# Optimization experiments

Measured on AMD Instinct MI355X. Metric: run time of the kernel, lower is better.

## Reference

```python
import jax, jax.numpy as jnp
import numpy as np

VOCAB, H, L, NUM_LABELS = 32000, 512, 5, 20


def setup_inputs() -> dict:
    key = jax.random.key(0)
    ks = jax.random.split(key, 8)
    B, T = 64, 512
    inputs = jax.random.randint(ks[0], (B, T), 0, VOCAB, dtype=jnp.int32)
    s = 1.0 / np.sqrt(H)
    emb = jax.random.normal(ks[1], (VOCAB, H), jnp.float32) * 0.02
    emb = emb.at[0].set(0.0)  # padding_idx=0
    W_ih = jax.random.uniform(ks[2], (L, 4 * H, H), jnp.float32, -s, s)
    W_hh = jax.random.uniform(ks[3], (L, 4 * H, H), jnp.float32, -s, s)
    b_ih = jax.random.uniform(ks[4], (L, 4 * H), jnp.float32, -s, s)
    b_hh = jax.random.uniform(ks[5], (L, 4 * H), jnp.float32, -s, s)
    W_cls = jax.random.uniform(ks[6], (NUM_LABELS, H), jnp.float32, -s, s)
    b_cls = jax.random.uniform(ks[7], (NUM_LABELS,), jnp.float32, -s, s)
    return {"inputs": inputs, "emb": emb, "W_ih": W_ih, "W_hh": W_hh,
            "b_ih": b_ih, "b_hh": b_hh, "W_cls": W_cls, "b_cls": b_cls}


def _lstm_layer(x, Wih, Whh, bih, bhh):
    # x: [B, T, H] -> [B, T, H]. PyTorch gate order: i, f, g, o.
    B, T, Hd = x.shape
    xg = jnp.einsum('bth,gh->btg', x, Wih) + bih + bhh  # precompute input gates [B,T,4H]

    def step(carry, xt):
        h, c = carry
        g = xt + h @ Whh.T
        i, f, gg, o = jnp.split(g, 4, axis=-1)
        c = jax.nn.sigmoid(f) * c + jax.nn.sigmoid(i) * jnp.tanh(gg)
        h = jax.nn.sigmoid(o) * jnp.tanh(c)
        return (h, c), h

    h0 = jnp.zeros((B, Hd), x.dtype)
    (_, _), ys = jax.lax.scan(step, (h0, h0), jnp.swapaxes(xg, 0, 1))
    return jnp.swapaxes(ys, 0, 1)


def reference(inputs, emb, W_ih, W_hh, b_ih, b_hh, W_cls, b_cls):
    # Dropout between layers is inactive in eval mode; omitted (deterministic baseline).
    x = emb[inputs]  # [B, T, H]
    for l in range(W_ih.shape[0]):
        x = _lstm_layer(x, W_ih[l], W_hh[l], b_ih[l], b_hh[l])
    feature = x[:, -1]  # last timestep hidden of top layer
    return feature @ W_cls.T + b_cls
```

## Files before the change

kernel.cpp:

```cpp
#include <hip/hip_runtime.h>
#include <cmath>

#define BB 64
#define TT 512
#define HH 512
#define GG 2048
#define TCH 64
#define LDT 132

template<bool GATHER>
__global__ __launch_bounds__(256) void xg_gemm(
    const float* __restrict__ Xsrc, const int* __restrict__ tok,
    const float* __restrict__ Wih, const float* __restrict__ bih,
    const float* __restrict__ bhh, float* __restrict__ XG, int t0)
{
  __shared__ float As[32 * LDT];
  __shared__ float Bs[32 * LDT];
  const int tid = threadIdx.x;
  const int tc = tid & 15, tr = tid >> 4;
  const int m0 = blockIdx.x * 128;
  const int g0 = blockIdx.y * 128;

  float acc[8][8];
#pragma unroll
  for (int i = 0; i < 8; ++i)
#pragma unroll
    for (int j = 0; j < 8; ++j) acc[i][j] = 0.f;

  float4 ra[4], rb[4];
#pragma unroll
  for (int i = 0; i < 4; ++i) {
    const int f = tid + i * 256;
    ra[i] = *(const float4*)&Wih[(size_t)(g0 + (f >> 3)) * HH + ((f & 7) << 2)];
  }
#pragma unroll
  for (int i = 0; i < 4; ++i) {
    const int f = tid + i * 256;
    if (GATHER) {
      const int m = m0 + (f >> 3);
      const int tok_i = tok[(m & 63) * TT + t0 + (m >> 6)];
      rb[i] = *(const float4*)&Xsrc[(size_t)tok_i * HH + ((f & 7) << 2)];
    } else {
      rb[i] = *(const float4*)&Xsrc[((size_t)(t0 + (m0 >> 6) + (f >> 9)) * HH
                                     + ((f >> 4) & 31)) * BB + ((f & 15) << 2)];
    }
  }

  for (int kt = 0; kt < 16; ++kt) {
#pragma unroll
    for (int i = 0; i < 4; ++i) {
      const int f = tid + i * 256;
      const int row = f >> 3, c4 = f & 7, s = c4 & 3;
      const int col = (((row >> 2) ^ s) << 2) + (row & 3);
      As[(c4 * 4 + 0) * LDT + col] = ra[i].x;
      As[(c4 * 4 + 1) * LDT + col] = ra[i].y;
      As[(c4 * 4 + 2) * LDT + col] = ra[i].z;
      As[(c4 * 4 + 3) * LDT + col] = ra[i].w;
    }
#pragma unroll
    for (int i = 0; i < 4; ++i) {
      const int f = tid + i * 256;
      if (GATHER) {
        const int row = f >> 3, c4 = f & 7, s = c4 & 3;
        const int col = (((row >> 2) ^ s) << 2) + (row & 3);
        Bs[(c4 * 4 + 0) * LDT + col] = rb[i].x;
        Bs[(c4 * 4 + 1) * LDT + col] = rb[i].y;
        Bs[(c4 * 4 + 2) * LDT + col] = rb[i].z;
        Bs[(c4 * 4 + 3) * LDT + col] = rb[i].w;
      } else {
        const int kk = (f >> 4) & 31, s = (kk >> 2) & 3;
        const int mq = (((f >> 9) << 4) + (f & 15)) ^ s;
        *(float4*)&Bs[kk * LDT + (mq << 2)] = rb[i];
      }
    }
    __syncthreads();
    if (kt < 15) {
      const int k0 = (kt + 1) * 32;
#pragma unroll
      for (int i = 0; i < 4; ++i) {
        const int f = tid + i * 256;
        ra[i] = *(const float4*)&Wih[(size_t)(g0 + (f >> 3)) * HH + k0 + ((f & 7) << 2)];
      }
#pragma unroll
      for (int i = 0; i < 4; ++i) {
        const int f = tid + i * 256;
        if (GATHER) {
          const int m = m0 + (f >> 3);
          const int tok_i = tok[(m & 63) * TT + t0 + (m >> 6)];
          rb[i] = *(const float4*)&Xsrc[(size_t)tok_i * HH + k0 + ((f & 7) << 2)];
        } else {
          rb[i] = *(const float4*)&Xsrc[((size_t)(t0 + (m0 >> 6) + (f >> 9)) * HH
                                         + k0 + ((f >> 4) & 31)) * BB + ((f & 15) << 2)];
        }
      }
    }
#pragma unroll
    for (int k = 0; k < 32; ++k) {
      const int s = (k >> 2) & 3;
      const float4 a0 = *(const float4*)&As[k * LDT + ((tr ^ s) << 2)];
      const float4 a1 = *(const float4*)&As[k * LDT + ((16 + (tr ^ s)) << 2)];
      const float4 b0 = *(const float4*)&Bs[k * LDT + ((tc ^ s) << 2)];
      const float4 b1 = *(const float4*)&Bs[k * LDT + ((16 + (tc ^ s)) << 2)];
      const float av[8] = {a0.x, a0.y, a0.z, a0.w, a1.x, a1.y, a1.z, a1.w};
      const float bv[8] = {b0.x, b0.y, b0.z, b0.w, b1.x, b1.y, b1.z, b1.w};
#pragma unroll
      for (int i2 = 0; i2 < 8; ++i2)
#pragma unroll
        for (int j2 = 0; j2 < 8; ++j2)
          acc[i2][j2] = fmaf(av[i2], bv[j2], acc[i2][j2]);
    }
    __syncthreads();
  }

#pragma unroll
  for (int ah = 0; ah < 2; ++ah)
#pragma unroll
    for (int i = 0; i < 4; ++i) {
      const int gc = g0 + ah * 64 + tr * 4 + i;
      const float bias = bih[gc] + bhh[gc];
#pragma unroll
      for (int bh = 0; bh < 2; ++bh) {
        const int tl_ = (m0 >> 6) + bh;
        float4 v;
        v.x = acc[ah * 4 + i][bh * 4 + 0] + bias;
        v.y = acc[ah * 4 + i][bh * 4 + 1] + bias;
        v.z = acc[ah * 4 + i][bh * 4 + 2] + bias;
        v.w = acc[ah * 4 + i][bh * 4 + 3] + bias;
        *(float4*)&XG[((size_t)tl_ * GG + gc) * BB + (tc << 2)] = v;
      }
    }
}

__device__ __forceinline__ float4 ld4a(const float* src) {
  const unsigned long long* p = (const unsigned long long*)src;
  const unsigned long long a = __hip_atomic_load(p + 0, __ATOMIC_RELAXED, __HIP_MEMORY_SCOPE_AGENT);
  const unsigned long long b = __hip_atomic_load(p + 1, __ATOMIC_RELAXED, __HIP_MEMORY_SCOPE_AGENT);
  float4 v;
  v.x = __uint_as_float((unsigned)a);
  v.y = __uint_as_float((unsigned)(a >> 32));
  v.z = __uint_as_float((unsigned)b);
  v.w = __uint_as_float((unsigned)(b >> 32));
  return v;
}

__global__ __launch_bounds__(256, 1) void lstm_chunk(
    const float* __restrict__ XG, const float* __restrict__ Whh,
    float* __restrict__ h0, float* __restrict__ h1,
    float* __restrict__ c, float* __restrict__ Y,
    unsigned* __restrict__ flag, int t0, int l)
{
  const int tid = threadIdx.x;
  const int grp = blockIdx.x & 7;
  const int mid = blockIdx.x >> 3;
  const int rp = tid >> 3;
  const int ks = tid & 7;
  const int lr0 = 2 * rp, lr1 = 2 * rp + 1;
  const int gc0 = ((lr0 >> 4) << 9) + mid * 16 + (lr0 & 15);
  const int gc1 = ((lr1 >> 4) << 9) + mid * 16 + (lr1 & 15);

  __shared__ float4 hs4[8 * 136];
  __shared__ float gs[512];

  float4 w0[16], w1[16];
#pragma unroll
  for (int cc = 0; cc < 16; ++cc) {
    w0[cc] = *(const float4*)&Whh[(size_t)gc0 * HH + ks * 64 + cc * 4];
    w1[cc] = *(const float4*)&Whh[(size_t)gc1 * HH + ks * 64 + cc * 4];
  }

  const int hc_l = tid >> 3;
  const int bb_l = tid & 7;
  const int hc_own = mid * 16 + hc_l;
  const int Bg_own = 8 * grp + bb_l;
  float creg = 0.f;
  if (t0 > 0 && tid < 128) creg = c[(size_t)hc_own * BB + Bg_own];

  const int sb = tid >> 7;
  const int sc4 = tid & 127;
  const int lds_i = sc4 + (sc4 >> 4);

  for (int tl = 0; tl < TCH; ++tl) {
    const int t = t0 + tl;
    const int first = (t == 0) ? 1 : 0;
    const float* h_in = (t & 1) ? h1 : h0;
    float* h_out = (t & 1) ? h0 : h1;

    float xgv[4];
    if (tid < 128) {
#pragma unroll
      for (int q = 0; q < 4; ++q)
        xgv[q] = XG[((size_t)tl * GG + (q << 9) + hc_own) * BB + Bg_own];
    }

    if (!first) {
      const float* s0 = &h_in[(size_t)(8 * grp + sb + 0) * HH + (sc4 << 2)];
      const float* s1 = &h_in[(size_t)(8 * grp + sb + 2) * HH + (sc4 << 2)];
      const float* s2 = &h_in[(size_t)(8 * grp + sb + 4) * HH + (sc4 << 2)];
      const float* s3 = &h_in[(size_t)(8 * grp + sb + 6) * HH + (sc4 << 2)];
      float4 va = ld4a(s0);
      float4 vb = ld4a(s1);
      hs4[(sb + 0) * 136 + lds_i] = va;
      va = ld4a(s2);
      hs4[(sb + 2) * 136 + lds_i] = vb;
      vb = ld4a(s3);
      hs4[(sb + 4) * 136 + lds_i] = va;
      hs4[(sb + 6) * 136 + lds_i] = vb;
      __syncthreads();

      float p0[8], p1[8];
#pragma unroll
      for (int b = 0; b < 8; ++b) { p0[b] = 0.f; p1[b] = 0.f; }
#pragma unroll
      for (int cc = 0; cc < 16; ++cc) {
#pragma unroll
        for (int b = 0; b < 8; ++b) {
          const float4 hv = hs4[b * 136 + 17 * ks + cc];
          p0[b] += hv.x * w0[cc].x + hv.y * w0[cc].y + hv.z * w0[cc].z + hv.w * w0[cc].w;
          p1[b] += hv.x * w1[cc].x + hv.y * w1[cc].y + hv.z * w1[cc].z + hv.w * w1[cc].w;
        }
      }
#pragma unroll
      for (int b = 0; b < 8; ++b) {
        float v0 = p0[b], v1 = p1[b];
        v0 += __shfl_xor(v0, 1, 64); v0 += __shfl_xor(v0, 2, 64); v0 += __shfl_xor(v0, 4, 64);
        v1 += __shfl_xor(v1, 1, 64); v1 += __shfl_xor(v1, 2, 64); v1 += __shfl_xor(v1, 4, 64);
        p0[b] = v0; p1[b] = v1;
      }
      if (ks == 0) {
#pragma unroll
        for (int b = 0; b < 8; ++b) {
          gs[lr0 * 8 + b] = p0[b];
          gs[lr1 * 8 + b] = p1[b];
        }
      }
    }
    __syncthreads();

    float hn = 0.f;
    if (tid < 128) {
      float gv[4];
#pragma unroll
      for (int q = 0; q < 4; ++q) {
        float x = xgv[q];
        if (!first) x += gs[(q * 16 + hc_l) * 8 + bb_l];
        gv[q] = x;
      }
      const float cold = first ? 0.f : creg;
      const float si = 1.f / (1.f + expf(-gv[0]));
      const float sf = 1.f / (1.f + expf(-gv[1]));
      const float so = 1.f / (1.f + expf(-gv[3]));
      const float cn = sf * cold + si * tanhf(gv[2]);
      hn = so * tanhf(cn);
      creg = cn;
      __hip_atomic_store(&h_out[(size_t)Bg_own * HH + hc_own], hn,
                         __ATOMIC_RELAXED, __HIP_MEMORY_SCOPE_AGENT);
    }

    asm volatile("s_waitcnt vmcnt(0)" ::: "memory");
    __syncthreads();
    const unsigned sid = (unsigned)(l * TT + t + 1);
    if (tid == 0)
      __hip_atomic_store(&flag[(grp << 5) + mid], sid,
                         __ATOMIC_RELAXED, __HIP_MEMORY_SCOPE_AGENT);
    if (tid < 128)
      Y[((size_t)t * HH + hc_own) * BB + Bg_own] = hn;
    if (tid < 32) {
      const unsigned* fp = &flag[(grp << 5) + tid];
      while (__hip_atomic_load(fp, __ATOMIC_RELAXED, __HIP_MEMORY_SCOPE_AGENT) < sid)
        __builtin_amdgcn_s_sleep(2);
    }
    __syncthreads();
  }

  if (tid < 128) c[(size_t)hc_own * BB + Bg_own] = creg;
}

__global__ __launch_bounds__(64) void cls_kernel(
    const float* __restrict__ Y, const float* __restrict__ Wcls,
    const float* __restrict__ bcls, float* __restrict__ out)
{
  __shared__ float feat[512];
  const int b = blockIdx.x, tid = threadIdx.x;
  for (int k = tid; k < HH; k += 64)
    feat[k] = Y[((size_t)(TT - 1) * HH + k) * BB + b];
  __syncthreads();
  if (tid < 20) {
    float acc = bcls[tid];
    for (int k = 0; k < HH; ++k) acc = fmaf(feat[k], Wcls[tid * HH + k], acc);
    out[b * 20 + tid] = acc;
  }
}

extern "C" void kernel_launch(void* const* d_in, const int* in_sizes, int n_in,
                              void* d_out, int out_size, void* d_ws, size_t ws_size,
                              hipStream_t stream) {
  (void)in_sizes; (void)n_in; (void)out_size; (void)ws_size;
  const int*   tok  = (const int*)d_in[0];
  const float* emb  = (const float*)d_in[1];
  const float* Wih  = (const float*)d_in[2];
  const float* Whh  = (const float*)d_in[3];
  const float* bih  = (const float*)d_in[4];
  const float* bhh  = (const float*)d_in[5];
  const float* Wcls = (const float*)d_in[6];
  const float* bcls = (const float*)d_in[7];
  float* out = (float*)d_out;

  float* Y  = (float*)d_ws;
  float* XG = Y + (size_t)TT * HH * BB;
  float* h0 = XG + (size_t)TCH * GG * BB;
  float* h1 = h0 + (size_t)BB * HH;
  float* c  = h1 + (size_t)BB * HH;
  unsigned* flag = (unsigned*)(c + (size_t)HH * BB);

  hipMemsetAsync(flag, 0, 256 * sizeof(unsigned), stream);

  for (int l = 0; l < 5; ++l) {
    const float* wih_l = Wih + (size_t)l * GG * HH;
    const float* whh_l = Whh + (size_t)l * GG * HH;
    const float* bih_l = bih + (size_t)l * GG;
    const float* bhh_l = bhh + (size_t)l * GG;
    for (int t0 = 0; t0 < TT; t0 += TCH) {
      if (l == 0)
        xg_gemm<true><<<dim3(32, 16), 256, 0, stream>>>(emb, tok, wih_l, bih_l, bhh_l, XG, t0);
      else
        xg_gemm<false><<<dim3(32, 16), 256, 0, stream>>>(Y, nullptr, wih_l, bih_l, bhh_l, XG, t0);
      lstm_chunk<<<256, 256, 0, stream>>>(XG, whh_l, h0, h1, c, Y, flag, t0, l);
    }
  }
  cls_kernel<<<64, 64, 0, stream>>>(Y, Wcls, bcls, out);
}
```

Measured before the change: 28.08 ms.

## Overlap next chunk's input-gate GEMM with current LSTM recurrence in one launch

Refactors the input-projection GEMM and the LSTM recurrence into device functions. A fused kernel runs 256 recurrence blocks for the current chunk plus 512 GEMM blocks that compute the next chunk's input gates into a second, double-buffered XG buffer. The goal is to hide the GEMM's serial time behind the latency-bound recurrence and to halve the number of launches. The fused path runs only when the workspace is large enough for two XG buffers. It relies on the recurrence blocks being dispatched first so their spin-wait barrier stays co-resident, and the GEMM blocks may compete with them for CU resources.

```diff
diff --git a/kernel.cpp b/kernel.cpp
--- a/kernel.cpp
+++ b/kernel.cpp
@@ -9,17 +9,16 @@
 #define LDT 132
 
 template<bool GATHER>
-__global__ __launch_bounds__(256) void xg_gemm(
+__device__ __forceinline__ void xg_body(
+    float* As, float* Bs,
     const float* __restrict__ Xsrc, const int* __restrict__ tok,
     const float* __restrict__ Wih, const float* __restrict__ bih,
-    const float* __restrict__ bhh, float* __restrict__ XG, int t0)
-{
-  __shared__ float As[32 * LDT];
-  __shared__ float Bs[32 * LDT];
-  const int tid = threadIdx.x;
+    const float* __restrict__ bhh, float* __restrict__ XG, int t0,
+    int bx, int by, int tid)
+{
   const int tc = tid & 15, tr = tid >> 4;
-  const int m0 = blockIdx.x * 128;
-  const int g0 = blockIdx.y * 128;
+  const int m0 = bx * 128;
+  const int g0 = by * 128;
 
   float acc[8][8];
 #pragma unroll
@@ -131,6 +130,18 @@
     }
 }
 
+template<bool GATHER>
+__global__ __launch_bounds__(256) void xg_gemm(
+    const float* __restrict__ Xsrc, const int* __restrict__ tok,
+    const float* __restrict__ Wih, const float* __restrict__ bih,
+    const float* __restrict__ bhh, float* __restrict__ XG, int t0)
+{
+  __shared__ float As[32 * LDT];
+  __shared__ float Bs[32 * LDT];
+  xg_body<GATHER>(As, Bs, Xsrc, tok, Wih, bih, bhh, XG, t0,
+                  blockIdx.x, blockIdx.y, threadIdx.x);
+}
+
 __device__ __forceinline__ float4 ld4a(const float* src) {
   const unsigned long long* p = (const unsigned long long*)src;
   const unsigned long long a = __hip_atomic_load(p + 0, __ATOMIC_RELAXED, __HIP_MEMORY_SCOPE_AGENT);
@@ -143,23 +154,20 @@
   return v;
 }
 
-__global__ __launch_bounds__(256, 1) void lstm_chunk(
+__device__ __forceinline__ void lstm_body(
+    float4* hs4, float* gs,
     const float* __restrict__ XG, const float* __restrict__ Whh,
     float* __restrict__ h0, float* __restrict__ h1,
     float* __restrict__ c, float* __restrict__ Y,
-    unsigned* __restrict__ flag, int t0, int l)
-{
-  const int tid = threadIdx.x;
-  const int grp = blockIdx.x & 7;
-  const int mid = blockIdx.x >> 3;
+    unsigned* __restrict__ flag, int t0, int l, int bid, int tid)
+{
+  const int grp = bid & 7;
+  const int mid = bid >> 3;
   const int rp = tid >> 3;
   const int ks = tid & 7;
   const int lr0 = 2 * rp, lr1 = 2 * rp + 1;
   const int gc0 = ((lr0 >> 4) << 9) + mid * 16 + (lr0 & 15);
   const int gc1 = ((lr1 >> 4) << 9) + mid * 16 + (lr1 & 15);
-
-  __shared__ float4 hs4[8 * 136];
-  __shared__ float gs[512];
 
   float4 w0[16], w1[16];
 #pragma unroll
@@ -275,6 +283,39 @@
   if (tid < 128) c[(size_t)hc_own * BB + Bg_own] = creg;
 }
 
+__global__ __launch_bounds__(256, 1) void lstm_chunk(
+    const float* __restrict__ XG, const float* __restrict__ Whh,
+    float* __restrict__ h0, float* __restrict__ h1,
+    float* __restrict__ c, float* __restrict__ Y,
+    unsigned* __restrict__ flag, int t0, int l)
+{
+  __shared__ float4 hs4[8 * 136];
+  __shared__ float gs[512];
+  lstm_body(hs4, gs, XG, Whh, h0, h1, c, Y, flag, t0, l, blockIdx.x, threadIdx.x);
+}
+
+template<bool GATHER>
+__global__ __launch_bounds__(256, 1) void fused_chunk(
+    const float* __restrict__ XGr, const float* __restrict__ Whh,
+    float* __restrict__ h0, float* __restrict__ h1,
+    float* __restrict__ cst, float* __restrict__ Y,
+    unsigned* __restrict__ flag, int t0, int l,
+    const float* __restrict__ Xsrc, const int* __restrict__ tok,
+    const float* __restrict__ Wih, const float* __restrict__ bih,
+    const float* __restrict__ bhh, float* __restrict__ XGw, int t0g)
+{
+  __shared__ float4 smem[2112];
+  if (blockIdx.x < 256) {
+    lstm_body(smem, (float*)(smem + 1088), XGr, Whh, h0, h1, cst, Y, flag,
+              t0, l, blockIdx.x, threadIdx.x);
+  } else {
+    const int b2 = blockIdx.x - 256;
+    xg_body<GATHER>((float*)smem, (float*)smem + 32 * LDT,
+                    Xsrc, tok, Wih, bih, bhh, XGw, t0g,
+                    b2 & 31, b2 >> 5, threadIdx.x);
+  }
+}
+
 __global__ __launch_bounds__(64) void cls_kernel(
     const float* __restrict__ Y, const float* __restrict__ Wcls,
     const float* __restrict__ bcls, float* __restrict__ out)
@@ -294,7 +335,7 @@
 extern "C" void kernel_launch(void* const* d_in, const int* in_sizes, int n_in,
                               void* d_out, int out_size, void* d_ws, size_t ws_size,
                               hipStream_t stream) {
-  (void)in_sizes; (void)n_in; (void)out_size; (void)ws_size;
+  (void)in_sizes; (void)n_in; (void)out_size;
   const int*   tok  = (const int*)d_in[0];
   const float* emb  = (const float*)d_in[1];
   const float* Wih  = (const float*)d_in[2];
@@ -305,26 +346,59 @@
   const float* bcls = (const float*)d_in[7];
   float* out = (float*)d_out;
 
-  float* Y  = (float*)d_ws;
-  float* XG = Y + (size_t)TT * HH * BB;
-  float* h0 = XG + (size_t)TCH * GG * BB;
-  float* h1 = h0 + (size_t)BB * HH;
-  float* c  = h1 + (size_t)BB * HH;
-  unsigned* flag = (unsigned*)(c + (size_t)HH * BB);
+  const size_t xgsz = (size_t)TCH * GG * BB;
+  const size_t need_ov = ((size_t)TT * HH * BB + 2 * xgsz + 3 * (size_t)BB * HH) * 4 + 1024;
+  const bool ov = ws_size >= need_ov;
+
+  float* Y   = (float*)d_ws;
+  float* XG0 = Y + (size_t)TT * HH * BB;
+  float* XG1 = ov ? XG0 + xgsz : XG0;
+  float* h0  = XG0 + (ov ? 2 : 1) * xgsz;
+  float* h1  = h0 + (size_t)BB * HH;
+  float* cst = h1 + (size_t)BB * HH;
+  unsigned* flag = (unsigned*)(cst + (size_t)HH * BB);
 
   hipMemsetAsync(flag, 0, 256 * sizeof(unsigned), stream);
 
-  for (int l = 0; l < 5; ++l) {
-    const float* wih_l = Wih + (size_t)l * GG * HH;
-    const float* whh_l = Whh + (size_t)l * GG * HH;
-    const float* bih_l = bih + (size_t)l * GG;
-    const float* bhh_l = bhh + (size_t)l * GG;
-    for (int t0 = 0; t0 < TT; t0 += TCH) {
-      if (l == 0)
-        xg_gemm<true><<<dim3(32, 16), 256, 0, stream>>>(emb, tok, wih_l, bih_l, bhh_l, XG, t0);
-      else
-        xg_gemm<false><<<dim3(32, 16), 256, 0, stream>>>(Y, nullptr, wih_l, bih_l, bhh_l, XG, t0);
-      lstm_chunk<<<256, 256, 0, stream>>>(XG, whh_l, h0, h1, c, Y, flag, t0, l);
+  if (ov) {
+    xg_gemm<true><<<dim3(32, 16), 256, 0, stream>>>(emb, tok, Wih, bih, bhh, XG0, 0);
+    for (int g = 0; g < 40; ++g) {
+      const int l = g >> 3, c = g & 7;
+      const float* whh_l = Whh + (size_t)l * GG * HH;
+      float* XGr = (g & 1) ? XG1 : XG0;
+      float* XGw = (g & 1) ? XG0 : XG1;
+      const int t0 = c * TCH;
+      if (g == 39) {
+        lstm_chunk<<<256, 256, 0, stream>>>(XGr, whh_l, h0, h1, cst, Y, flag, t0, l);
+      } else {
+        const int gn = g + 1, ln = gn >> 3, cn = gn & 7;
+        const float* wih_n = Wih + (size_t)ln * GG * HH;
+        const float* bih_n = bih + (size_t)ln * GG;
+        const float* bhh_n = bhh + (size_t)ln * GG;
+        const int t0g = cn * TCH;
+        if (ln == 0)
+          fused_chunk<true><<<768, 256, 0, stream>>>(
+              XGr, whh_l, h0, h1, cst, Y, flag, t0, l,
+              emb, tok, wih_n, bih_n, bhh_n, XGw, t0g);
+        else
+          fused_chunk<false><<<768, 256, 0, stream>>>(
+              XGr, whh_l, h0, h1, cst, Y, flag, t0, l,
+              Y, nullptr, wih_n, bih_n, bhh_n, XGw, t0g);
+      }
+    }
+  } else {
+    for (int l = 0; l < 5; ++l) {
+      const float* wih_l = Wih + (size_t)l * GG * HH;
+      const float* whh_l = Whh + (size_t)l * GG * HH;
+      const float* bih_l = bih + (size_t)l * GG;
+      const float* bhh_l = bhh + (size_t)l * GG;
+      for (int t0 = 0; t0 < TT; t0 += TCH) {
+        if (l == 0)
+          xg_gemm<true><<<dim3(32, 16), 256, 0, stream>>>(emb, tok, wih_l, bih_l, bhh_l, XG0, t0);
+        else
+          xg_gemm<false><<<dim3(32, 16), 256, 0, stream>>>(Y, nullptr, wih_l, bih_l, bhh_l, XG0, t0);
+        lstm_chunk<<<256, 256, 0, stream>>>(XG0, whh_l, h0, h1, cst, Y, flag, t0, l);
+      }
     }
   }
   cls_kernel<<<64, 64, 0, stream>>>(Y, Wcls, bcls, out);
```

New measurement: 27.81 ms. About the same (-0.9%).
